# Optimization experiments

Hardware: AMD Instinct MI355X
Metric: run time of the kernel (lower is better)

The kernel has to match this reference:

```python
import jax, jax.numpy as jnp
import numpy as np

MARGIN = 0.3
BATCH = 4096
FEAT = 256
NUM_IDS = 512


def setup_inputs() -> dict:
    key = jax.random.key(0)
    k1, k2 = jax.random.split(key)
    features = jax.random.normal(k1, (BATCH, FEAT), dtype=jnp.float32)
    labels = jax.random.randint(k2, (BATCH,), 0, NUM_IDS, dtype=jnp.int64 if jax.config.jax_enable_x64 else jnp.int32)
    return {"features": features, "labels": labels}


def reference(features, labels):
    n = features.shape[0]
    sq_norm = jnp.sum(features * features, axis=-1)  # [n]
    sq = sq_norm[:, None] + sq_norm[None, :] - 2.0 * (features @ features.T)
    dist = jnp.sqrt(jnp.maximum(sq, 1e-12))  # [n, n], == torch.cdist p=2

    same = labels[:, None] == labels[None, :]           # [n, n]
    eye = jnp.eye(n, dtype=bool)
    pos_mask = same & ~eye
    neg_mask = ~same

    NEG_INF = jnp.float32(-1e30)
    POS_INF = jnp.float32(1e30)
    hard_pos = jnp.max(jnp.where(pos_mask, dist, NEG_INF), axis=1)  # [n]
    hard_neg = jnp.min(jnp.where(neg_mask, dist, POS_INF), axis=1)  # [n]

    valid = pos_mask.any(axis=1) & neg_mask.any(axis=1)
    row_loss = jnp.maximum(hard_pos - hard_neg + MARGIN, 0.0)
    count = jnp.sum(valid)
    total = jnp.sum(jnp.where(valid, row_loss, 0.0))
    return jnp.where(count > 0, total / jnp.maximum(count, 1).astype(total.dtype), jnp.float32(0.0))
```

## Files before the change

### kernel.cpp

```cpp
#include <hip/hip_runtime.h>

typedef unsigned short ushort_t;
typedef __attribute__((ext_vector_type(8))) short bf16x8;
typedef __attribute__((ext_vector_type(4))) float f32x4;

#define NROWS 4096
#define DIM   256
#define MARGINF 0.3f

__device__ __forceinline__ unsigned enc_f(float f) {
  unsigned u = __float_as_uint(f);
  return (u & 0x80000000u) ? ~u : (u | 0x80000000u);
}
__device__ __forceinline__ float dec_f(unsigned k) {
  unsigned u = (k & 0x80000000u) ? (k ^ 0x80000000u) : ~k;
  return __uint_as_float(u);
}

__device__ __forceinline__ ushort_t f2b(float f) {
  unsigned u = __float_as_uint(f);
  u += 0x7fffu + ((u >> 16) & 1u);
  return (ushort_t)(u >> 16);
}

__device__ __forceinline__ void gload_lds16(const void* g, void* l) {
  __builtin_amdgcn_global_load_lds(
      (const __attribute__((address_space(1))) void*)g,
      (__attribute__((address_space(3))) void*)l, 16, 0, 0);
}

__global__ void k_prep(const float* __restrict__ F, ushort_t* __restrict__ Fb,
                       float* __restrict__ nrm, unsigned* __restrict__ posk,
                       unsigned* __restrict__ negk) {
  const int tid = threadIdx.x;
  const int wave = tid >> 6, lane = tid & 63;
  const int row = blockIdx.x * 4 + wave;

  const float4 v = *(const float4*)&F[row * DIM + lane * 4];
  float s = fmaf(v.x, v.x, fmaf(v.y, v.y, fmaf(v.z, v.z, v.w * v.w)));
  #pragma unroll
  for (int off = 32; off; off >>= 1) s += __shfl_down(s, off);
  if (lane == 0) nrm[row] = s;

  ushort4 o;
  o.x = f2b(v.x); o.y = f2b(v.y); o.z = f2b(v.z); o.w = f2b(v.w);
  *(ushort4*)&Fb[row * DIM + lane * 4] = o;

  const int gid = blockIdx.x * 256 + tid;
  if (gid < NROWS) { posk[gid] = enc_f(-1e30f); negk[gid] = enc_f(1e30f); }
}

__global__ __launch_bounds__(256, 2) void k_gram(
    const ushort_t* __restrict__ Fb, const int* __restrict__ lab,
    const float* __restrict__ nrm,
    unsigned* __restrict__ posk, unsigned* __restrict__ negk) {
  __shared__ alignas(16) ushort_t As[128 * 32];
  __shared__ alignas(16) ushort_t Bs[128 * 32];
  __shared__ int labi[128], labj[128];
  __shared__ float nrmi[128], nrmj[128];
  __shared__ float redp[2][128], redn[2][128];

  const int tid = threadIdx.x;
  const int wave = tid >> 6, lane = tid & 63;
  const int wm = wave >> 1, wn = wave & 1;
  const int rt = blockIdx.x & 31, ct = blockIdx.x >> 5;
  const int row0 = rt * 128, col0 = ct * 128;

  if (tid < 128) { labi[tid] = lab[row0 + tid]; nrmi[tid] = nrm[row0 + tid]; }
  else { int t = tid - 128; labj[t] = lab[col0 + t]; nrmj[t] = nrm[col0 + t]; }

  f32x4 acc[4][4];
  #pragma unroll
  for (int m = 0; m < 4; ++m)
    #pragma unroll
    for (int n = 0; n < 4; ++n) acc[m][n] = (f32x4){0.f, 0.f, 0.f, 0.f};

  const int lrow = lane >> 2;
  const int lcol = (lane & 3) * 8;

  for (int kk = 0; kk < 8; ++kk) {
    #pragma unroll
    for (int s = 0; s < 2; ++s) {
      const int rbase = s * 64 + wave * 16;
      gload_lds16(&Fb[(row0 + rbase + lrow) * DIM + kk * 32 + lcol], &As[rbase * 32]);
      gload_lds16(&Fb[(col0 + rbase + lrow) * DIM + kk * 32 + lcol], &Bs[rbase * 32]);
    }
    __syncthreads();

    bf16x8 a[4], b[4];
    #pragma unroll
    for (int m = 0; m < 4; ++m)
      a[m] = *(const bf16x8*)&As[(wm * 64 + m * 16 + (lane & 15)) * 32 + (lane >> 4) * 8];
    #pragma unroll
    for (int n = 0; n < 4; ++n)
      b[n] = *(const bf16x8*)&Bs[(wn * 64 + n * 16 + (lane & 15)) * 32 + (lane >> 4) * 8];
    #pragma unroll
    for (int m = 0; m < 4; ++m)
      #pragma unroll
      for (int n = 0; n < 4; ++n)
        acc[m][n] = __builtin_amdgcn_mfma_f32_16x16x32_bf16(a[m], b[n], acc[m][n], 0, 0, 0);
    __syncthreads();
  }

  const int h = lane >> 4, ccol = lane & 15;
  float posr[4][4], negr[4][4];
  #pragma unroll
  for (int m = 0; m < 4; ++m)
    #pragma unroll
    for (int j = 0; j < 4; ++j) { posr[m][j] = -1e30f; negr[m][j] = 1e30f; }

  #pragma unroll
  for (int m = 0; m < 4; ++m) {
    #pragma unroll
    for (int n = 0; n < 4; ++n) {
      const int cl = wn * 64 + n * 16 + ccol;
      const float nj = nrmj[cl];
      const int lj = labj[cl];
      #pragma unroll
      for (int j = 0; j < 4; ++j) {
        const int rl = wm * 64 + m * 16 + h * 4 + j;
        const float sq = nrmi[rl] + nj - 2.f * acc[m][n][j];
        const bool same = (labi[rl] == lj);
        if (same) {
          if (row0 + rl != col0 + cl) posr[m][j] = fmaxf(posr[m][j], sq);
        } else {
          negr[m][j] = fminf(negr[m][j], sq);
        }
      }
    }
  }

  #pragma unroll
  for (int m = 0; m < 4; ++m) {
    #pragma unroll
    for (int j = 0; j < 4; ++j) {
      float p = posr[m][j], q = negr[m][j];
      #pragma unroll
      for (int mask = 1; mask <= 8; mask <<= 1) {
        p = fmaxf(p, __shfl_xor(p, mask));
        q = fminf(q, __shfl_xor(q, mask));
      }
      if (ccol == 0) {
        const int rl = wm * 64 + m * 16 + h * 4 + j;
        redp[wn][rl] = p; redn[wn][rl] = q;
      }
    }
  }
  __syncthreads();
  if (tid < 128) {
    const float p = fmaxf(redp[0][tid], redp[1][tid]);
    const float q = fminf(redn[0][tid], redn[1][tid]);
    atomicMax(&posk[row0 + tid], enc_f(p));
    atomicMin(&negk[row0 + tid], enc_f(q));
  }
}

__global__ void k_final(const unsigned* __restrict__ posk,
                        const unsigned* __restrict__ negk,
                        float* __restrict__ out) {
  int t = threadIdx.x;
  float sum = 0.f;
  int cnt = 0;
  for (int i = t; i < NROWS; i += 1024) {
    float ps = dec_f(posk[i]);
    float ns = dec_f(negk[i]);
    if ((ps > -1e29f) && (ns < 1e29f)) {
      float hp = sqrtf(fmaxf(ps, 1e-12f));
      float hn = sqrtf(fmaxf(ns, 1e-12f));
      sum += fmaxf(hp - hn + MARGINF, 0.f);
      cnt += 1;
    }
  }
  #pragma unroll
  for (int off = 32; off; off >>= 1) {
    sum += __shfl_down(sum, off);
    cnt += __shfl_down(cnt, off);
  }
  __shared__ float wsum[16];
  __shared__ int wcnt[16];
  int w = t >> 6;
  if ((t & 63) == 0) { wsum[w] = sum; wcnt[w] = cnt; }
  __syncthreads();
  if (t == 0) {
    float S = 0.f; int C = 0;
    #pragma unroll
    for (int i = 0; i < 16; ++i) { S += wsum[i]; C += wcnt[i]; }
    out[0] = (C > 0) ? (S / (float)C) : 0.f;
  }
}

extern "C" void kernel_launch(void* const* d_in, const int* in_sizes, int n_in,
                              void* d_out, int out_size, void* d_ws, size_t ws_size,
                              hipStream_t stream) {
  const float* F = (const float*)d_in[0];
  const int* lab = (const int*)d_in[1];
  float* out = (float*)d_out;

  unsigned* posk = (unsigned*)d_ws;
  unsigned* negk = posk + NROWS;
  float* nrm = (float*)(negk + NROWS);
  ushort_t* Fb = (ushort_t*)(nrm + NROWS);

  k_prep<<<NROWS / 4, 256, 0, stream>>>(F, Fb, nrm, posk, negk);
  k_gram<<<32 * 32, 256, 0, stream>>>(Fb, lab, nrm, posk, negk);
  k_final<<<1, 1024, 0, stream>>>(posk, negk, out);
}
```

Baseline: 80.73 us.

## Exploit distance symmetry with triangular tiles, double-buffered LDS, and slot-based reductions

Because the distance matrix is symmetric, the Gram kernel now launches only the upper-triangular 128x128 tile pairs. Each tile produces both row-wise and column-wise hard-positive and hard-negative values, which roughly halves the MFMA and epilogue work. The K loop double-buffers the LDS tiles so the next slice's global-to-LDS load is issued before the current slice's MFMAs. Global atomics on encoded keys are replaced by per-tile slot writes, reduced later by a new two-stage final kernel. The costs are an extra kernel launch, more epilogue shuffles, twice the LDS, and a larger workspace.

```diff
diff --git a/kernel.cpp b/kernel.cpp
--- a/kernel.cpp
+++ b/kernel.cpp
@@ -6,16 +6,8 @@
 
 #define NROWS 4096
 #define DIM   256
+#define NT    32
 #define MARGINF 0.3f
-
-__device__ __forceinline__ unsigned enc_f(float f) {
-  unsigned u = __float_as_uint(f);
-  return (u & 0x80000000u) ? ~u : (u | 0x80000000u);
-}
-__device__ __forceinline__ float dec_f(unsigned k) {
-  unsigned u = (k & 0x80000000u) ? (k ^ 0x80000000u) : ~k;
-  return __uint_as_float(u);
-}
 
 __device__ __forceinline__ ushort_t f2b(float f) {
   unsigned u = __float_as_uint(f);
@@ -30,8 +22,7 @@
 }
 
 __global__ void k_prep(const float* __restrict__ F, ushort_t* __restrict__ Fb,
-                       float* __restrict__ nrm, unsigned* __restrict__ posk,
-                       unsigned* __restrict__ negk) {
+                       float* __restrict__ nrm) {
   const int tid = threadIdx.x;
   const int wave = tid >> 6, lane = tid & 63;
   const int row = blockIdx.x * 4 + wave;
@@ -45,26 +36,28 @@
   ushort4 o;
   o.x = f2b(v.x); o.y = f2b(v.y); o.z = f2b(v.z); o.w = f2b(v.w);
   *(ushort4*)&Fb[row * DIM + lane * 4] = o;
-
-  const int gid = blockIdx.x * 256 + tid;
-  if (gid < NROWS) { posk[gid] = enc_f(-1e30f); negk[gid] = enc_f(1e30f); }
 }
 
 __global__ __launch_bounds__(256, 2) void k_gram(
     const ushort_t* __restrict__ Fb, const int* __restrict__ lab,
     const float* __restrict__ nrm,
-    unsigned* __restrict__ posk, unsigned* __restrict__ negk) {
-  __shared__ alignas(16) ushort_t As[128 * 32];
-  __shared__ alignas(16) ushort_t Bs[128 * 32];
+    float* __restrict__ pslot, float* __restrict__ nslot) {
+  __shared__ alignas(16) ushort_t As[2][128 * 32];
+  __shared__ alignas(16) ushort_t Bs[2][128 * 32];
   __shared__ int labi[128], labj[128];
   __shared__ float nrmi[128], nrmj[128];
   __shared__ float redp[2][128], redn[2][128];
+  __shared__ float redpc[2][128], rednc[2][128];
 
   const int tid = threadIdx.x;
   const int wave = tid >> 6, lane = tid & 63;
   const int wm = wave >> 1, wn = wave & 1;
-  const int rt = blockIdx.x & 31, ct = blockIdx.x >> 5;
+
+  int rem = blockIdx.x, rt = 0;
+  while (rem >= NT - rt) { rem -= NT - rt; ++rt; }
+  const int ct = rt + rem;
   const int row0 = rt * 128, col0 = ct * 128;
+  const bool isdiag = (rt == ct);
 
   if (tid < 128) { labi[tid] = lab[row0 + tid]; nrmi[tid] = nrm[row0 + tid]; }
   else { int t = tid - 128; labj[t] = lab[col0 + t]; nrmj[t] = nrm[col0 + t]; }
@@ -78,22 +71,32 @@
   const int lrow = lane >> 2;
   const int lcol = (lane & 3) * 8;
 
+  #pragma unroll
+  for (int s = 0; s < 2; ++s) {
+    const int rbase = s * 64 + wave * 16;
+    gload_lds16(&Fb[(row0 + rbase + lrow) * DIM + lcol], &As[0][rbase * 32]);
+    gload_lds16(&Fb[(col0 + rbase + lrow) * DIM + lcol], &Bs[0][rbase * 32]);
+  }
+  __syncthreads();
+
   for (int kk = 0; kk < 8; ++kk) {
-    #pragma unroll
-    for (int s = 0; s < 2; ++s) {
-      const int rbase = s * 64 + wave * 16;
-      gload_lds16(&Fb[(row0 + rbase + lrow) * DIM + kk * 32 + lcol], &As[rbase * 32]);
-      gload_lds16(&Fb[(col0 + rbase + lrow) * DIM + kk * 32 + lcol], &Bs[rbase * 32]);
-    }
-    __syncthreads();
-
+    const int cur = kk & 1;
+    if (kk < 7) {
+      const int nxt = cur ^ 1;
+      #pragma unroll
+      for (int s = 0; s < 2; ++s) {
+        const int rbase = s * 64 + wave * 16;
+        gload_lds16(&Fb[(row0 + rbase + lrow) * DIM + (kk + 1) * 32 + lcol], &As[nxt][rbase * 32]);
+        gload_lds16(&Fb[(col0 + rbase + lrow) * DIM + (kk + 1) * 32 + lcol], &Bs[nxt][rbase * 32]);
+      }
+    }
     bf16x8 a[4], b[4];
     #pragma unroll
     for (int m = 0; m < 4; ++m)
-      a[m] = *(const bf16x8*)&As[(wm * 64 + m * 16 + (lane & 15)) * 32 + (lane >> 4) * 8];
+      a[m] = *(const bf16x8*)&As[cur][(wm * 64 + m * 16 + (lane & 15)) * 32 + (lane >> 4) * 8];
     #pragma unroll
     for (int n = 0; n < 4; ++n)
-      b[n] = *(const bf16x8*)&Bs[(wn * 64 + n * 16 + (lane & 15)) * 32 + (lane >> 4) * 8];
+      b[n] = *(const bf16x8*)&Bs[cur][(wn * 64 + n * 16 + (lane & 15)) * 32 + (lane >> 4) * 8];
     #pragma unroll
     for (int m = 0; m < 4; ++m)
       #pragma unroll
@@ -104,10 +107,13 @@
 
   const int h = lane >> 4, ccol = lane & 15;
   float posr[4][4], negr[4][4];
+  float posc[4], negc[4];
   #pragma unroll
   for (int m = 0; m < 4; ++m)
     #pragma unroll
     for (int j = 0; j < 4; ++j) { posr[m][j] = -1e30f; negr[m][j] = 1e30f; }
+  #pragma unroll
+  for (int n = 0; n < 4; ++n) { posc[n] = -1e30f; negc[n] = 1e30f; }
 
   #pragma unroll
   for (int m = 0; m < 4; ++m) {
@@ -121,10 +127,15 @@
         const int rl = wm * 64 + m * 16 + h * 4 + j;
         const float sq = nrmi[rl] + nj - 2.f * acc[m][n][j];
         const bool same = (labi[rl] == lj);
+        const bool self = isdiag && (rl == cl);
         if (same) {
-          if (row0 + rl != col0 + cl) posr[m][j] = fmaxf(posr[m][j], sq);
+          if (!self) {
+            posr[m][j] = fmaxf(posr[m][j], sq);
+            posc[n] = fmaxf(posc[n], sq);
+          }
         } else {
           negr[m][j] = fminf(negr[m][j], sq);
+          negc[n] = fminf(negc[n], sq);
         }
       }
     }
@@ -146,47 +157,80 @@
       }
     }
   }
+  #pragma unroll
+  for (int n = 0; n < 4; ++n) {
+    float p = posc[n], q = negc[n];
+    #pragma unroll
+    for (int mask = 16; mask <= 32; mask <<= 1) {
+      p = fmaxf(p, __shfl_xor(p, mask));
+      q = fminf(q, __shfl_xor(q, mask));
+    }
+    if (lane < 16) {
+      redpc[wm][wn * 64 + n * 16 + lane] = p;
+      rednc[wm][wn * 64 + n * 16 + lane] = q;
+    }
+  }
   __syncthreads();
+
   if (tid < 128) {
     const float p = fmaxf(redp[0][tid], redp[1][tid]);
     const float q = fminf(redn[0][tid], redn[1][tid]);
-    atomicMax(&posk[row0 + tid], enc_f(p));
-    atomicMin(&negk[row0 + tid], enc_f(q));
-  }
-}
-
-__global__ void k_final(const unsigned* __restrict__ posk,
-                        const unsigned* __restrict__ negk,
-                        float* __restrict__ out) {
-  int t = threadIdx.x;
-  float sum = 0.f;
-  int cnt = 0;
-  for (int i = t; i < NROWS; i += 1024) {
-    float ps = dec_f(posk[i]);
-    float ns = dec_f(negk[i]);
-    if ((ps > -1e29f) && (ns < 1e29f)) {
-      float hp = sqrtf(fmaxf(ps, 1e-12f));
-      float hn = sqrtf(fmaxf(ns, 1e-12f));
-      sum += fmaxf(hp - hn + MARGINF, 0.f);
-      cnt += 1;
-    }
-  }
+    pslot[ct * NROWS + row0 + tid] = p;
+    nslot[ct * NROWS + row0 + tid] = q;
+    if (!isdiag) {
+      const float pc = fmaxf(redpc[0][tid], redpc[1][tid]);
+      const float qc = fminf(rednc[0][tid], rednc[1][tid]);
+      pslot[rt * NROWS + col0 + tid] = pc;
+      nslot[rt * NROWS + col0 + tid] = qc;
+    }
+  }
+}
+
+__global__ void k_final1(const float* __restrict__ pslot,
+                         const float* __restrict__ nslot,
+                         float* __restrict__ bsum, float* __restrict__ bcnt) {
+  const int tid = threadIdx.x;
+  const int row = blockIdx.x * 128 + tid;
+  float p = -1e30f, q = 1e30f;
+  #pragma unroll
+  for (int s = 0; s < NT; ++s) {
+    p = fmaxf(p, pslot[s * NROWS + row]);
+    q = fminf(q, nslot[s * NROWS + row]);
+  }
+  float loss = 0.f, cnt = 0.f;
+  if ((p > -1e29f) && (q < 1e29f)) {
+    const float hp = sqrtf(fmaxf(p, 1e-12f));
+    const float hn = sqrtf(fmaxf(q, 1e-12f));
+    loss = fmaxf(hp - hn + MARGINF, 0.f);
+    cnt = 1.f;
+  }
+  const int lane = tid & 63;
   #pragma unroll
   for (int off = 32; off; off >>= 1) {
-    sum += __shfl_down(sum, off);
+    loss += __shfl_down(loss, off);
     cnt += __shfl_down(cnt, off);
   }
-  __shared__ float wsum[16];
-  __shared__ int wcnt[16];
-  int w = t >> 6;
-  if ((t & 63) == 0) { wsum[w] = sum; wcnt[w] = cnt; }
+  __shared__ float ws[2], wc[2];
+  if (lane == 0) { ws[tid >> 6] = loss; wc[tid >> 6] = cnt; }
   __syncthreads();
-  if (t == 0) {
-    float S = 0.f; int C = 0;
-    #pragma unroll
-    for (int i = 0; i < 16; ++i) { S += wsum[i]; C += wcnt[i]; }
-    out[0] = (C > 0) ? (S / (float)C) : 0.f;
-  }
+  if (tid == 0) {
+    bsum[blockIdx.x] = ws[0] + ws[1];
+    bcnt[blockIdx.x] = wc[0] + wc[1];
+  }
+}
+
+__global__ void k_final2(const float* __restrict__ bsum,
+                         const float* __restrict__ bcnt,
+                         float* __restrict__ out) {
+  const int lane = threadIdx.x;
+  float s = (lane < NT) ? bsum[lane] : 0.f;
+  float c = (lane < NT) ? bcnt[lane] : 0.f;
+  #pragma unroll
+  for (int off = 32; off; off >>= 1) {
+    s += __shfl_down(s, off);
+    c += __shfl_down(c, off);
+  }
+  if (lane == 0) out[0] = (c > 0.f) ? (s / c) : 0.f;
 }
 
 extern "C" void kernel_launch(void* const* d_in, const int* in_sizes, int n_in,
@@ -196,12 +240,15 @@
   const int* lab = (const int*)d_in[1];
   float* out = (float*)d_out;
 
-  unsigned* posk = (unsigned*)d_ws;
-  unsigned* negk = posk + NROWS;
-  float* nrm = (float*)(negk + NROWS);
-  ushort_t* Fb = (ushort_t*)(nrm + NROWS);
-
-  k_prep<<<NROWS / 4, 256, 0, stream>>>(F, Fb, nrm, posk, negk);
-  k_gram<<<32 * 32, 256, 0, stream>>>(Fb, lab, nrm, posk, negk);
-  k_final<<<1, 1024, 0, stream>>>(posk, negk, out);
-}
+  float* pslot = (float*)d_ws;
+  float* nslot = pslot + NT * NROWS;
+  float* nrm = nslot + NT * NROWS;
+  float* bsum = nrm + NROWS;
+  float* bcnt = bsum + NT;
+  ushort_t* Fb = (ushort_t*)(bcnt + NT);
+
+  k_prep<<<NROWS / 4, 256, 0, stream>>>(F, Fb, nrm);
+  k_gram<<<NT * (NT + 1) / 2, 256, 0, stream>>>(Fb, lab, nrm, pslot, nslot);
+  k_final1<<<NT, 128, 0, stream>>>(pslot, nslot, bsum, bcnt);
+  k_final2<<<1, 64, 0, stream>>>(bsum, bcnt, out);
+}
```

Result: slower. 88.84 us (+10.0%).

## Exploit Gram symmetry with upper-triangular tiles and double-buffer LDS loads

Applied to the files above, without the earlier changes.

The Gram kernel now launches only upper-triangular tile pairs (528 instead of 1024 blocks). Each off-diagonal tile also reduces along columns and updates the mined extrema for the column rows, so the symmetric half of the matrix is never computed. The K loop is double-buffered in LDS so the next slice loads while MFMAs run on the current one, and launch bounds ask for 3 blocks per CU. In exchange it adds column reduction work, more atomics per tile, a serial loop to map block index to tile, and more shared memory per block.

```diff
diff --git a/kernel.cpp b/kernel.cpp
--- a/kernel.cpp
+++ b/kernel.cpp
@@ -6,6 +6,7 @@
 
 #define NROWS 4096
 #define DIM   256
+#define NT    32
 #define MARGINF 0.3f
 
 __device__ __forceinline__ unsigned enc_f(float f) {
@@ -50,21 +51,26 @@
   if (gid < NROWS) { posk[gid] = enc_f(-1e30f); negk[gid] = enc_f(1e30f); }
 }
 
-__global__ __launch_bounds__(256, 2) void k_gram(
+__global__ __launch_bounds__(256, 3) void k_gram(
     const ushort_t* __restrict__ Fb, const int* __restrict__ lab,
     const float* __restrict__ nrm,
     unsigned* __restrict__ posk, unsigned* __restrict__ negk) {
-  __shared__ alignas(16) ushort_t As[128 * 32];
-  __shared__ alignas(16) ushort_t Bs[128 * 32];
+  __shared__ alignas(16) ushort_t As[2][128 * 32];
+  __shared__ alignas(16) ushort_t Bs[2][128 * 32];
   __shared__ int labi[128], labj[128];
   __shared__ float nrmi[128], nrmj[128];
   __shared__ float redp[2][128], redn[2][128];
+  __shared__ float redpc[2][128], rednc[2][128];
 
   const int tid = threadIdx.x;
   const int wave = tid >> 6, lane = tid & 63;
   const int wm = wave >> 1, wn = wave & 1;
-  const int rt = blockIdx.x & 31, ct = blockIdx.x >> 5;
+
+  int rem = blockIdx.x, rt = 0;
+  while (rem >= NT - rt) { rem -= NT - rt; ++rt; }
+  const int ct = rt + rem;
   const int row0 = rt * 128, col0 = ct * 128;
+  const bool isdiag = (rt == ct);
 
   if (tid < 128) { labi[tid] = lab[row0 + tid]; nrmi[tid] = nrm[row0 + tid]; }
   else { int t = tid - 128; labj[t] = lab[col0 + t]; nrmj[t] = nrm[col0 + t]; }
@@ -78,22 +84,32 @@
   const int lrow = lane >> 2;
   const int lcol = (lane & 3) * 8;
 
+  #pragma unroll
+  for (int s = 0; s < 2; ++s) {
+    const int rbase = s * 64 + wave * 16;
+    gload_lds16(&Fb[(row0 + rbase + lrow) * DIM + lcol], &As[0][rbase * 32]);
+    gload_lds16(&Fb[(col0 + rbase + lrow) * DIM + lcol], &Bs[0][rbase * 32]);
+  }
+  __syncthreads();
+
   for (int kk = 0; kk < 8; ++kk) {
-    #pragma unroll
-    for (int s = 0; s < 2; ++s) {
-      const int rbase = s * 64 + wave * 16;
-      gload_lds16(&Fb[(row0 + rbase + lrow) * DIM + kk * 32 + lcol], &As[rbase * 32]);
-      gload_lds16(&Fb[(col0 + rbase + lrow) * DIM + kk * 32 + lcol], &Bs[rbase * 32]);
-    }
-    __syncthreads();
-
+    const int cur = kk & 1;
+    if (kk < 7) {
+      const int nxt = cur ^ 1;
+      #pragma unroll
+      for (int s = 0; s < 2; ++s) {
+        const int rbase = s * 64 + wave * 16;
+        gload_lds16(&Fb[(row0 + rbase + lrow) * DIM + (kk + 1) * 32 + lcol], &As[nxt][rbase * 32]);
+        gload_lds16(&Fb[(col0 + rbase + lrow) * DIM + (kk + 1) * 32 + lcol], &Bs[nxt][rbase * 32]);
+      }
+    }
     bf16x8 a[4], b[4];
     #pragma unroll
     for (int m = 0; m < 4; ++m)
-      a[m] = *(const bf16x8*)&As[(wm * 64 + m * 16 + (lane & 15)) * 32 + (lane >> 4) * 8];
+      a[m] = *(const bf16x8*)&As[cur][(wm * 64 + m * 16 + (lane & 15)) * 32 + (lane >> 4) * 8];
     #pragma unroll
     for (int n = 0; n < 4; ++n)
-      b[n] = *(const bf16x8*)&Bs[(wn * 64 + n * 16 + (lane & 15)) * 32 + (lane >> 4) * 8];
+      b[n] = *(const bf16x8*)&Bs[cur][(wn * 64 + n * 16 + (lane & 15)) * 32 + (lane >> 4) * 8];
     #pragma unroll
     for (int m = 0; m < 4; ++m)
       #pragma unroll
@@ -104,10 +120,13 @@
 
   const int h = lane >> 4, ccol = lane & 15;
   float posr[4][4], negr[4][4];
+  float posc[4], negc[4];
   #pragma unroll
   for (int m = 0; m < 4; ++m)
     #pragma unroll
     for (int j = 0; j < 4; ++j) { posr[m][j] = -1e30f; negr[m][j] = 1e30f; }
+  #pragma unroll
+  for (int n = 0; n < 4; ++n) { posc[n] = -1e30f; negc[n] = 1e30f; }
 
   #pragma unroll
   for (int m = 0; m < 4; ++m) {
@@ -121,10 +140,15 @@
         const int rl = wm * 64 + m * 16 + h * 4 + j;
         const float sq = nrmi[rl] + nj - 2.f * acc[m][n][j];
         const bool same = (labi[rl] == lj);
+        const bool self = isdiag && (rl == cl);
         if (same) {
-          if (row0 + rl != col0 + cl) posr[m][j] = fmaxf(posr[m][j], sq);
+          if (!self) {
+            posr[m][j] = fmaxf(posr[m][j], sq);
+            posc[n] = fmaxf(posc[n], sq);
+          }
         } else {
           negr[m][j] = fminf(negr[m][j], sq);
+          negc[n] = fminf(negc[n], sq);
         }
       }
     }
@@ -146,12 +170,32 @@
       }
     }
   }
+  #pragma unroll
+  for (int n = 0; n < 4; ++n) {
+    float p = posc[n], q = negc[n];
+    #pragma unroll
+    for (int mask = 16; mask <= 32; mask <<= 1) {
+      p = fmaxf(p, __shfl_xor(p, mask));
+      q = fminf(q, __shfl_xor(q, mask));
+    }
+    if (lane < 16) {
+      redpc[wm][wn * 64 + n * 16 + lane] = p;
+      rednc[wm][wn * 64 + n * 16 + lane] = q;
+    }
+  }
   __syncthreads();
+
   if (tid < 128) {
     const float p = fmaxf(redp[0][tid], redp[1][tid]);
     const float q = fminf(redn[0][tid], redn[1][tid]);
     atomicMax(&posk[row0 + tid], enc_f(p));
     atomicMin(&negk[row0 + tid], enc_f(q));
+    if (!isdiag) {
+      const float pc = fmaxf(redpc[0][tid], redpc[1][tid]);
+      const float qc = fminf(rednc[0][tid], rednc[1][tid]);
+      atomicMax(&posk[col0 + tid], enc_f(pc));
+      atomicMin(&negk[col0 + tid], enc_f(qc));
+    }
   }
 }
 
@@ -202,6 +246,6 @@
   ushort_t* Fb = (ushort_t*)(nrm + NROWS);
 
   k_prep<<<NROWS / 4, 256, 0, stream>>>(F, Fb, nrm, posk, negk);
-  k_gram<<<32 * 32, 256, 0, stream>>>(Fb, lab, nrm, posk, negk);
+  k_gram<<<NT * (NT + 1) / 2, 256, 0, stream>>>(Fb, lab, nrm, posk, negk);
   k_final<<<1, 1024, 0, stream>>>(posk, negk, out);
 }
```

Result: no change. 80.05 us (-0.8%).
